# Kernel tuning notes

Hardware: AMD Instinct MI355X
Metric: run time of the kernel (lower is better)

## Reference

```python
import jax, jax.numpy as jnp
import numpy as np

N_NODES = 90
RATIO = 0.5
K = int(np.ceil(RATIO * N_NODES))  # 45


def setup_inputs() -> dict:
    key = jax.random.key(0)
    k1, k2, k3, k4, k5 = jax.random.split(key, 5)
    B, D = 512, 1024  # D = 4 * num_features
    x_sc = jax.random.normal(k1, (B, N_NODES, D), dtype=jnp.float32)
    x_fc = jax.random.normal(k2, (B, N_NODES, D), dtype=jnp.float32)
    # uniform(size, w): U(-1/sqrt(size), 1/sqrt(size))
    b_pool = 1.0 / np.sqrt(D)
    pool_w = jax.random.uniform(k3, (D, 1), minval=-b_pool, maxval=b_pool, dtype=jnp.float32)
    b_mw = 1.0 / np.sqrt(2.0)
    multi_w = jax.random.uniform(k4, (2, 1), minval=-b_mw, maxval=b_mw, dtype=jnp.float32)
    b_mb = 1.0 / np.sqrt(N_NODES)
    multi_b = jax.random.uniform(k5, (N_NODES,), minval=-b_mb, maxval=b_mb, dtype=jnp.float32)
    return {"x_sc": x_sc, "x_fc": x_fc, "pool_w": pool_w, "multi_w": multi_w, "multi_b": multi_b}


def reference(x_sc, x_fc, pool_w, multi_w, multi_b):
    B, N, D = x_sc.shape  # N == 90

    def pool_score(x):  # PoolScore: tanh((x @ w) / ||w||_2)
        s = jnp.einsum('bnd,do->bn', x, pool_w)
        return jnp.tanh(s / jnp.linalg.norm(pool_w))

    sc_score = pool_score(x_sc)  # [B, N]
    fc_score = pool_score(x_fc)  # [B, N]
    all_score = jnp.stack((sc_score, fc_score), axis=-1)  # [B, N, 2]
    multi_score = jax.nn.sigmoid(jnp.einsum('bnc,co->bn', all_score, multi_w) + multi_b)  # [B, N]

    # topk: sort descending, keep first K indices
    node_index = jnp.argsort(-multi_score, axis=1)[:, :K]  # [B, K]

    w = multi_score[:, :, None]  # [B, N, 1]
    wx_sc = x_sc * w
    wx_fc = x_fc * w
    idx = node_index[:, :, None]  # [B, K, 1]
    select_wx_sc = jnp.take_along_axis(wx_sc, jnp.broadcast_to(idx, (B, K, D)), axis=1)
    select_wx_fc = jnp.take_along_axis(wx_fc, jnp.broadcast_to(idx, (B, K, D)), axis=1)
    return select_wx_sc, select_wx_fc
```

## Files before the change

### kernel.cpp

```cpp
#include <hip/hip_runtime.h>
#include <math.h>

#define N_NODES 90
#define KSEL 45
#define DIM 1024
#define BATCH 512

__global__ __launch_bounds__(256) void score_kernel(
    const float* __restrict__ x_sc, const float* __restrict__ x_fc,
    const float* __restrict__ pool_w, const float* __restrict__ multi_w,
    const float* __restrict__ multi_b, float* __restrict__ scores)
{
    const int row = blockIdx.x;
    const int tid = threadIdx.x;
    const size_t base = (size_t)row * DIM;

    const float4* a4 = (const float4*)(x_sc + base);
    const float4* b4 = (const float4*)(x_fc + base);
    const float4* w4 = (const float4*)pool_w;

    float4 a = a4[tid];
    float4 b = b4[tid];
    float4 w = w4[tid];

    float dsc = a.x*w.x + a.y*w.y + a.z*w.z + a.w*w.w;
    float dfc = b.x*w.x + b.y*w.y + b.z*w.z + b.w*w.w;
    float wsq = w.x*w.x + w.y*w.y + w.z*w.z + w.w*w.w;

    for (int off = 32; off > 0; off >>= 1) {
        dsc += __shfl_down(dsc, off, 64);
        dfc += __shfl_down(dfc, off, 64);
        wsq += __shfl_down(wsq, off, 64);
    }

    __shared__ float s1[4], s2[4], s3[4];
    const int wave = tid >> 6, lane = tid & 63;
    if (lane == 0) { s1[wave] = dsc; s2[wave] = dfc; s3[wave] = wsq; }
    __syncthreads();

    if (tid == 0) {
        float t1 = s1[0] + s1[1] + s1[2] + s1[3];
        float t2 = s2[0] + s2[1] + s2[2] + s2[3];
        float t3 = s3[0] + s3[1] + s3[2] + s3[3];
        float inv_norm = rsqrtf(t3);
        float sc = tanhf(t1 * inv_norm);
        float fc = tanhf(t2 * inv_norm);
        int n = row % N_NODES;
        float z = sc * multi_w[0] + fc * multi_w[1] + multi_b[n];
        scores[row] = 1.0f / (1.0f + expf(-z));
    }
}

__global__ __launch_bounds__(128) void topk_kernel(
    const float* __restrict__ scores, int* __restrict__ idx,
    float* __restrict__ wgt)
{
    const int b = blockIdx.x;
    const int t = threadIdx.x;
    __shared__ float s[N_NODES];
    if (t < N_NODES) s[t] = scores[b * N_NODES + t];
    __syncthreads();
    if (t < N_NODES) {
        float v = s[t];
        int rank = 0;
        #pragma unroll
        for (int j = 0; j < N_NODES; ++j) {
            float u = s[j];
            rank += (u > v) || (u == v && j < t);
        }
        if (rank < KSEL) {
            idx[b * KSEL + rank] = t;
            wgt[b * KSEL + rank] = v;
        }
    }
}

__global__ __launch_bounds__(256) void gather_kernel(
    const float* __restrict__ x_sc, const float* __restrict__ x_fc,
    const int* __restrict__ idx, const float* __restrict__ wgt,
    float* __restrict__ out)
{
    const int m = blockIdx.x;
    const int b = m / KSEL;
    const int t = threadIdx.x;

    const int n = idx[m];
    const float w = wgt[m];

    const size_t src = ((size_t)b * N_NODES + n) * DIM;
    const size_t dst = (size_t)m * DIM;

    const float4* a4 = (const float4*)(x_sc + src);
    const float4* b4 = (const float4*)(x_fc + src);
    float4* o1 = (float4*)(out + dst);
    float4* o2 = (float4*)(out + (size_t)BATCH * KSEL * DIM + dst);

    float4 a = a4[t];
    a.x *= w; a.y *= w; a.z *= w; a.w *= w;
    o1[t] = a;
    float4 c = b4[t];
    c.x *= w; c.y *= w; c.z *= w; c.w *= w;
    o2[t] = c;
}

extern "C" void kernel_launch(void* const* d_in, const int* in_sizes, int n_in,
                              void* d_out, int out_size, void* d_ws, size_t ws_size,
                              hipStream_t stream) {
    const float* x_sc    = (const float*)d_in[0];
    const float* x_fc    = (const float*)d_in[1];
    const float* pool_w  = (const float*)d_in[2];
    const float* multi_w = (const float*)d_in[3];
    const float* multi_b = (const float*)d_in[4];
    float* out = (float*)d_out;

    float* scores = (float*)d_ws;
    float* wgt    = scores + BATCH * N_NODES;
    int*   idx    = (int*)(wgt + BATCH * KSEL);

    score_kernel<<<BATCH * N_NODES, 256, 0, stream>>>(
        x_sc, x_fc, pool_w, multi_w, multi_b, scores);
    topk_kernel<<<BATCH, 128, 0, stream>>>(scores, idx, wgt);
    gather_kernel<<<BATCH * KSEL, 256, 0, stream>>>(
        x_sc, x_fc, idx, wgt, out);
}
```

Before: 462.7 us.

## Use one wave per row with grid-stride loops in score and gather kernels

The score and gather kernels now assign one 64-lane wavefront per row, and each lane handles four float4s. Persistent grid-stride loops replace the one-block-per-row launch. In the score kernel this removes the shared-memory cross-wave reduction and __syncthreads, and it computes the pool_w norm once per wave instead of once per row. The goal is less block launch and synchronization overhead and more memory requests in flight per thread for these bandwidth-bound passes, at the cost of higher register use and fixed grid sizes.

```diff
diff --git a/kernel.cpp b/kernel.cpp
--- a/kernel.cpp
+++ b/kernel.cpp
@@ -5,49 +5,52 @@
 #define KSEL 45
 #define DIM 1024
 #define BATCH 512
+#define NROWS (BATCH * N_NODES)
+#define MROWS (BATCH * KSEL)
+
+#define DOT4(p, q) ((p).x*(q).x + (p).y*(q).y + (p).z*(q).z + (p).w*(q).w)
 
 __global__ __launch_bounds__(256) void score_kernel(
     const float* __restrict__ x_sc, const float* __restrict__ x_fc,
     const float* __restrict__ pool_w, const float* __restrict__ multi_w,
     const float* __restrict__ multi_b, float* __restrict__ scores)
 {
-    const int row = blockIdx.x;
-    const int tid = threadIdx.x;
-    const size_t base = (size_t)row * DIM;
+    const int lane = threadIdx.x & 63;
+    const int wid  = (blockIdx.x << 2) | (threadIdx.x >> 6);
+    const int nw   = gridDim.x << 2;
 
-    const float4* a4 = (const float4*)(x_sc + base);
-    const float4* b4 = (const float4*)(x_fc + base);
     const float4* w4 = (const float4*)pool_w;
+    const float4 w0 = w4[lane], w1 = w4[64 + lane],
+                 w2 = w4[128 + lane], w3 = w4[192 + lane];
 
-    float4 a = a4[tid];
-    float4 b = b4[tid];
-    float4 w = w4[tid];
+    float wsq = DOT4(w0, w0) + DOT4(w1, w1) + DOT4(w2, w2) + DOT4(w3, w3);
+    #pragma unroll
+    for (int off = 32; off; off >>= 1) wsq += __shfl_down(wsq, off, 64);
+    const float inv_norm = rsqrtf(__shfl(wsq, 0, 64));
+    const float mw0 = multi_w[0], mw1 = multi_w[1];
 
-    float dsc = a.x*w.x + a.y*w.y + a.z*w.z + a.w*w.w;
-    float dfc = b.x*w.x + b.y*w.y + b.z*w.z + b.w*w.w;
-    float wsq = w.x*w.x + w.y*w.y + w.z*w.z + w.w*w.w;
+    for (int row = wid; row < NROWS; row += nw) {
+        const float4* a4 = (const float4*)(x_sc + (size_t)row * DIM);
+        const float4* b4 = (const float4*)(x_fc + (size_t)row * DIM);
+        float4 a0 = a4[lane], a1 = a4[64 + lane],
+               a2 = a4[128 + lane], a3 = a4[192 + lane];
+        float4 c0 = b4[lane], c1 = b4[64 + lane],
+               c2 = b4[128 + lane], c3 = b4[192 + lane];
 
-    for (int off = 32; off > 0; off >>= 1) {
-        dsc += __shfl_down(dsc, off, 64);
-        dfc += __shfl_down(dfc, off, 64);
-        wsq += __shfl_down(wsq, off, 64);
-    }
+        float dsc = DOT4(a0, w0) + DOT4(a1, w1) + DOT4(a2, w2) + DOT4(a3, w3);
+        float dfc = DOT4(c0, w0) + DOT4(c1, w1) + DOT4(c2, w2) + DOT4(c3, w3);
 
-    __shared__ float s1[4], s2[4], s3[4];
-    const int wave = tid >> 6, lane = tid & 63;
-    if (lane == 0) { s1[wave] = dsc; s2[wave] = dfc; s3[wave] = wsq; }
-    __syncthreads();
-
-    if (tid == 0) {
-        float t1 = s1[0] + s1[1] + s1[2] + s1[3];
-        float t2 = s2[0] + s2[1] + s2[2] + s2[3];
-        float t3 = s3[0] + s3[1] + s3[2] + s3[3];
-        float inv_norm = rsqrtf(t3);
-        float sc = tanhf(t1 * inv_norm);
-        float fc = tanhf(t2 * inv_norm);
-        int n = row % N_NODES;
-        float z = sc * multi_w[0] + fc * multi_w[1] + multi_b[n];
-        scores[row] = 1.0f / (1.0f + expf(-z));
+        #pragma unroll
+        for (int off = 32; off; off >>= 1) {
+            dsc += __shfl_down(dsc, off, 64);
+            dfc += __shfl_down(dfc, off, 64);
+        }
+        if (lane == 0) {
+            float sc = tanhf(dsc * inv_norm);
+            float fc = tanhf(dfc * inv_norm);
+            float z = sc * mw0 + fc * mw1 + multi_b[row % N_NODES];
+            scores[row] = 1.0f / (1.0f + expf(-z));
+        }
     }
 }
 
@@ -80,27 +83,39 @@
     const int* __restrict__ idx, const float* __restrict__ wgt,
     float* __restrict__ out)
 {
-    const int m = blockIdx.x;
-    const int b = m / KSEL;
-    const int t = threadIdx.x;
+    const int lane = threadIdx.x & 63;
+    const int wid  = (blockIdx.x << 2) | (threadIdx.x >> 6);
+    const int nw   = gridDim.x << 2;
+    const size_t OUT2 = (size_t)MROWS * DIM;
 
-    const int n = idx[m];
-    const float w = wgt[m];
+    for (int m = wid; m < MROWS; m += nw) {
+        const int b = m / KSEL;
+        const int n = idx[m];
+        const float w = wgt[m];
+        const size_t src = ((size_t)b * N_NODES + n) * DIM;
 
-    const size_t src = ((size_t)b * N_NODES + n) * DIM;
-    const size_t dst = (size_t)m * DIM;
+        const float4* a4 = (const float4*)(x_sc + src);
+        const float4* b4 = (const float4*)(x_fc + src);
+        float4* o1 = (float4*)(out + (size_t)m * DIM);
+        float4* o2 = (float4*)(out + OUT2 + (size_t)m * DIM);
 
-    const float4* a4 = (const float4*)(x_sc + src);
-    const float4* b4 = (const float4*)(x_fc + src);
-    float4* o1 = (float4*)(out + dst);
-    float4* o2 = (float4*)(out + (size_t)BATCH * KSEL * DIM + dst);
+        float4 a0 = a4[lane], a1 = a4[64 + lane],
+               a2 = a4[128 + lane], a3 = a4[192 + lane];
+        float4 c0 = b4[lane], c1 = b4[64 + lane],
+               c2 = b4[128 + lane], c3 = b4[192 + lane];
 
-    float4 a = a4[t];
-    a.x *= w; a.y *= w; a.z *= w; a.w *= w;
-    o1[t] = a;
-    float4 c = b4[t];
-    c.x *= w; c.y *= w; c.z *= w; c.w *= w;
-    o2[t] = c;
+        a0.x *= w; a0.y *= w; a0.z *= w; a0.w *= w;
+        a1.x *= w; a1.y *= w; a1.z *= w; a1.w *= w;
+        a2.x *= w; a2.y *= w; a2.z *= w; a2.w *= w;
+        a3.x *= w; a3.y *= w; a3.z *= w; a3.w *= w;
+        c0.x *= w; c0.y *= w; c0.z *= w; c0.w *= w;
+        c1.x *= w; c1.y *= w; c1.z *= w; c1.w *= w;
+        c2.x *= w; c2.y *= w; c2.z *= w; c2.w *= w;
+        c3.x *= w; c3.y *= w; c3.z *= w; c3.w *= w;
+
+        o1[lane] = a0; o1[64 + lane] = a1; o1[128 + lane] = a2; o1[192 + lane] = a3;
+        o2[lane] = c0; o2[64 + lane] = c1; o2[128 + lane] = c2; o2[192 + lane] = c3;
+    }
 }
 
 extern "C" void kernel_launch(void* const* d_in, const int* in_sizes, int n_in,
@@ -117,9 +132,9 @@
     float* wgt    = scores + BATCH * N_NODES;
     int*   idx    = (int*)(wgt + BATCH * KSEL);
 
-    score_kernel<<<BATCH * N_NODES, 256, 0, stream>>>(
+    score_kernel<<<2880, 256, 0, stream>>>(
         x_sc, x_fc, pool_w, multi_w, multi_b, scores);
     topk_kernel<<<BATCH, 128, 0, stream>>>(scores, idx, wgt);
-    gather_kernel<<<BATCH * KSEL, 256, 0, stream>>>(
+    gather_kernel<<<1440, 256, 0, stream>>>(
         x_sc, x_fc, idx, wgt, out);
 }
```

Result: slower. 477.8 us (+3.2%).
